# Optimization experiments

Hardware: AMD Instinct MI355X
Metric: run time of the kernel (lower is better)

Reference implementation:

```python
import jax, jax.numpy as jnp
import numpy as np

B = 262144          # flattened batch of (sample, time) points
D = 16              # input_dim: number of independent per-dimension MLPs
TE = 3              # time_embedding_dim -> per-dim MLP input width = 1 + TE = 4
H = 64              # hidden width (model_dims = [64, 64, 1])


def setup_inputs() -> dict:
    key = jax.random.key(0)
    ks = jax.random.split(key, 8)
    s1 = 1.0 / np.sqrt(1 + TE)   # torch nn.Linear default init scale ~ U(-1/sqrt(fan_in), ...)
    s2 = 1.0 / np.sqrt(H)
    return {
        "t": jax.random.normal(ks[0], (B, TE), jnp.float32),
        "y": jax.random.normal(ks[1], (B, D), jnp.float32),
        # stacked per-dim weights: layer l weight [D, in_l, out_l], bias [D, out_l]
        "W1": jax.random.uniform(ks[2], (D, 1 + TE, H), jnp.float32, -s1, s1),
        "b1": jax.random.uniform(ks[3], (D, H), jnp.float32, -s1, s1),
        "W2": jax.random.uniform(ks[4], (D, H, H), jnp.float32, -s2, s2),
        "b2": jax.random.uniform(ks[5], (D, H), jnp.float32, -s2, s2),
        "W3": jax.random.uniform(ks[6], (D, H, 1), jnp.float32, -s2, s2),
        "b3": jax.random.uniform(ks[7], (D, 1), jnp.float32, -s2, s2),
    }


def reference(t, y, W1, b1, W2, b2, W3, b3):
    # Per-dim MLP input: concat([y_i, t]) -> [B, D, 1+TE]
    Bn, Dn = y.shape
    x = jnp.concatenate(
        [y[:, :, None], jnp.broadcast_to(t[:, None, :], (Bn, Dn, t.shape[-1]))], axis=-1
    )
    h = jax.nn.softplus(jnp.einsum("bdi,dih->bdh", x, W1) + b1)      # Linear + Softplus
    h = jax.nn.softplus(jnp.einsum("bdh,dhk->bdk", h, W2) + b2)      # Linear + Softplus
    out = jnp.einsum("bdk,dko->bdo", h, W3) + b3                      # final Linear, out=1
    # concat over D then final activation: [B, D]
    return jax.nn.softplus(out[..., 0])
```

## Files before the change

kernel.cpp:

```cpp
#include <hip/hip_runtime.h>
#include <cmath>

#define B_TOTAL 262144
#define D 16
#define TE 3
#define H 64

#define TPB 16
#define NBX (B_TOTAL / 16 / TPB)
#define NBY 4

#define LOG2E 1.44269504088896340736f
#define LN2   0.693147180559945309417f

#define RSH 72
#define ARS 10

#define OSTRIDE (TPB * 16 * 4)

typedef _Float16 half8  __attribute__((ext_vector_type(8)));
typedef _Float16 half4  __attribute__((ext_vector_type(4)));
typedef __fp16   fp16x2 __attribute__((ext_vector_type(2)));
typedef float    f32x4  __attribute__((ext_vector_type(4)));
typedef unsigned int uint32;

__device__ __forceinline__ float sp_log2(float xs) {
    return __builtin_amdgcn_logf(1.0f + __builtin_amdgcn_exp2f(xs));
}
__device__ __forceinline__ float softplus_full(float x) {
    float e = __builtin_amdgcn_exp2f(-fabsf(x) * LOG2E);
    return fmaxf(x, 0.0f) + LN2 * __builtin_amdgcn_logf(1.0f + e);
}

__global__ __launch_bounds__(256, 4) void DiagonalVariance_kernel(
    const float* __restrict__ t,
    const float* __restrict__ y,
    const float* __restrict__ W1,
    const float* __restrict__ b1,
    const float* __restrict__ W2,
    const float* __restrict__ b2,
    const float* __restrict__ W3,
    const float* __restrict__ b3,
    float* __restrict__ out)
{
    __shared__ __align__(16) _Float16 tbuf[4 * 16 * RSH];
    __shared__ __align__(16) float obuf[2 * OSTRIDE];
    __shared__ __align__(16) uint32 abuf[256 * ARS];

    const int wave = threadIdx.x >> 6;
    const int lane = threadIdx.x & 63;
    const int q    = lane >> 4;
    const int lm   = lane & 15;
    const int d    = blockIdx.y * 4 + wave;
    const bool q0  = (q == 0);

    {
        const int i    = threadIdx.x;
        const int grow = blockIdx.x * 256 + i;
        const f32x4 yv = *(const f32x4*)(y + grow * D + blockIdx.y * 4);
        const float* tpp = t + grow * TE;
        const float tt0 = tpp[0], tt1 = tpp[1], tt2 = tpp[2];
        const uint32 u1 = __builtin_bit_cast(uint32, __builtin_amdgcn_cvt_pkrtz(tt1, tt2));
        uint32* ab = abuf + i * ARS;
        ab[0] = __builtin_bit_cast(uint32, __builtin_amdgcn_cvt_pkrtz(yv.x, tt0)); ab[1] = u1;
        ab[2] = __builtin_bit_cast(uint32, __builtin_amdgcn_cvt_pkrtz(yv.y, tt0)); ab[3] = u1;
        ab[4] = __builtin_bit_cast(uint32, __builtin_amdgcn_cvt_pkrtz(yv.z, tt0)); ab[5] = u1;
        ab[6] = __builtin_bit_cast(uint32, __builtin_amdgcn_cvt_pkrtz(yv.w, tt0)); ab[7] = u1;
    }

    const float* __restrict__ W1d = W1 + d * (4 * H);
    const float* __restrict__ b1d = b1 + d * H;
    const float* __restrict__ W2d = W2 + d * (H * H);
    const float* __restrict__ b2d = b2 + d * H;
    const float* __restrict__ W3d = W3 + d * H;

    half8 w2f[2][4];
    #pragma unroll
    for (int ks = 0; ks < 2; ++ks)
        #pragma unroll
        for (int nt = 0; nt < 4; ++nt)
            #pragma unroll
            for (int j = 0; j < 8; ++j)
                w2f[ks][nt][j] = (_Float16)W2d[(32 * ks + 8 * q + j) * H + 16 * nt + lm];

    half4 w1f[4];
    #pragma unroll
    for (int nt = 0; nt < 4; ++nt) {
        #pragma unroll
        for (int i = 0; i < 4; ++i) {
            const int h = 16 * nt + lm;
            float v = 0.0f;
            if (q == 0)           v = W1d[i * H + h] * LOG2E;
            if (q == 1 && i == 0) v = b1d[h] * LOG2E;
            w1f[nt][i] = (_Float16)v;
        }
    }

    const f32x4 ZC = {0.f, 0.f, 0.f, 0.f};
    f32x4 b2c[4];
    #pragma unroll
    for (int nt = 0; nt < 4; ++nt) {
        f32x4 bv = *(const f32x4*)(b2d + 16 * nt + 4 * q);
        b2c[nt] = (f32x4){bv.x * LOG2E, bv.y * LOG2E, bv.z * LOG2E, bv.w * LOG2E};
    }

    f32x4 w3l[4];
    #pragma unroll
    for (int nt = 0; nt < 4; ++nt) {
        f32x4 wv = *(const f32x4*)(W3d + 16 * nt + 4 * q);
        w3l[nt] = (f32x4){wv.x * LN2, wv.y * LN2, wv.z * LN2, wv.w * LN2};
    }

    const float sInit = ((lane & 48) == 0) ? b3[d] : 0.0f;

    _Float16* const tb  = tbuf + wave * (16 * RSH);
    _Float16* const twr = tb + (q * 4) * RSH + lm;
    const _Float16* const trd = tb + lm * RSH + 8 * q;

    const uint32* const ard = abuf + lm * ARS + 2 * wave;

    __syncthreads();

    uint32 a0n = ard[0];
    uint32 a1n = ard[1];

    #pragma unroll 1
    for (int tg = 0; tg < TPB; ++tg) {
        const uint32 a0 = a0n;
        const uint32 a1 = a1n;
        {
            const int tn = (tg + 1 < TPB) ? (tg + 1) : tg;
            a0n = ard[tn * 16 * ARS + 0];
            a1n = ard[tn * 16 * ARS + 1];
        }
        union { half4 h; uint32 u[2]; } af;
        af.u[0] = q0 ? a0 : 0x00003C00u;
        af.u[1] = q0 ? a1 : 0u;

        f32x4 acc1[4];
        #pragma unroll
        for (int nt = 0; nt < 4; ++nt)
            acc1[nt] = __builtin_amdgcn_mfma_f32_16x16x16f16(af.h, w1f[nt], ZC, 0, 0, 0);

        #pragma unroll
        for (int nt = 0; nt < 4; ++nt) {
            const fp16x2 p01 = __builtin_amdgcn_cvt_pkrtz(sp_log2(acc1[nt][0]),
                                                          sp_log2(acc1[nt][1]));
            const fp16x2 p23 = __builtin_amdgcn_cvt_pkrtz(sp_log2(acc1[nt][2]),
                                                          sp_log2(acc1[nt][3]));
            __fp16* const wb = (__fp16*)(twr + nt * 16);
            wb[0 * RSH] = p01.x;
            wb[1 * RSH] = p01.y;
            wb[2 * RSH] = p23.x;
            wb[3 * RSH] = p23.y;
        }

        half8 a2[2];
        #pragma unroll
        for (int ks = 0; ks < 2; ++ks)
            a2[ks] = *(const half8*)(trd + 32 * ks);

        f32x4 acc2[4];
        #pragma unroll
        for (int nt = 0; nt < 4; ++nt)
            acc2[nt] = __builtin_amdgcn_mfma_f32_16x16x32_f16(w2f[0][nt], a2[0], b2c[nt], 0, 0, 0);
        #pragma unroll
        for (int nt = 0; nt < 4; ++nt)
            acc2[nt] = __builtin_amdgcn_mfma_f32_16x16x32_f16(w2f[1][nt], a2[1], acc2[nt], 0, 0, 0);

        float s0 = sInit, s1 = 0.0f;
        #pragma unroll
        for (int nt = 0; nt < 4; ++nt) {
            s0 = fmaf(sp_log2(acc2[nt][0]), w3l[nt][0], s0);
            s1 = fmaf(sp_log2(acc2[nt][1]), w3l[nt][1], s1);
            s0 = fmaf(sp_log2(acc2[nt][2]), w3l[nt][2], s0);
            s1 = fmaf(sp_log2(acc2[nt][3]), w3l[nt][3], s1);
        }
        float s = s0 + s1;
        const uint32 sw = (uint32)__builtin_amdgcn_ds_swizzle(
            (int)__builtin_bit_cast(uint32, s), 0x401F);
        s += __builtin_bit_cast(float, sw);
        if ((lane & 16) == 0)
            obuf[(lane >> 5) * OSTRIDE + (tg * 16 + lm) * 4 + wave] = s;
    }

    __syncthreads();
    const int i = threadIdx.x;
    const f32x4 va = *(const f32x4*)(obuf + 4 * i);
    const f32x4 vb = *(const f32x4*)(obuf + OSTRIDE + 4 * i);
    f32x4 v;
    v.x = softplus_full(va.x + vb.x);
    v.y = softplus_full(va.y + vb.y);
    v.z = softplus_full(va.z + vb.z);
    v.w = softplus_full(va.w + vb.w);
    *(f32x4*)(out + (blockIdx.x * 256 + i) * D + blockIdx.y * 4) = v;
}

extern "C" void kernel_launch(void* const* d_in, const int* in_sizes, int n_in,
                              void* d_out, int out_size, void* d_ws, size_t ws_size,
                              hipStream_t stream) {
    const float* t  = (const float*)d_in[0];
    const float* y  = (const float*)d_in[1];
    const float* W1 = (const float*)d_in[2];
    const float* b1 = (const float*)d_in[3];
    const float* W2 = (const float*)d_in[4];
    const float* b2 = (const float*)d_in[5];
    const float* W3 = (const float*)d_in[6];
    const float* b3 = (const float*)d_in[7];
    float* out = (float*)d_out;

    DiagonalVariance_kernel<<<dim3(NBX, NBY), dim3(256), 0, stream>>>(
        t, y, W1, b1, W2, b2, W3, b3, out);
}
```

Before: 192.6 us.

## Keep layer-1 activations in registers by transposing MFMA to remove LDS round-trip

Layer 1 now computes the transposed product (weights as A, inputs as B), so each lane's accumulator output already sits in the B-operand layout a 16x16x16 MFMA expects. The hidden activations are packed to fp16 in registers and fed straight into layer 2, which removes the per-iteration LDS write/read through tbuf along with that buffer. Layer 2 moves from 8 K=32 MFMAs to 16 K=16 MFMAs, with W2 re-laid out to match. The trade-off is more MFMA issues per tile in exchange for dropping the shared-memory traffic and its waits.

```diff
diff --git a/kernel.cpp b/kernel.cpp
--- a/kernel.cpp
+++ b/kernel.cpp
@@ -13,7 +13,6 @@
 #define LOG2E 1.44269504088896340736f
 #define LN2   0.693147180559945309417f
 
-#define RSH 72
 #define ARS 10
 
 #define OSTRIDE (TPB * 16 * 4)
@@ -43,7 +42,6 @@
     const float* __restrict__ b3,
     float* __restrict__ out)
 {
-    __shared__ __align__(16) _Float16 tbuf[4 * 16 * RSH];
     __shared__ __align__(16) float obuf[2 * OSTRIDE];
     __shared__ __align__(16) uint32 abuf[256 * ARS];
 
@@ -74,15 +72,6 @@
     const float* __restrict__ b2d = b2 + d * H;
     const float* __restrict__ W3d = W3 + d * H;
 
-    half8 w2f[2][4];
-    #pragma unroll
-    for (int ks = 0; ks < 2; ++ks)
-        #pragma unroll
-        for (int nt = 0; nt < 4; ++nt)
-            #pragma unroll
-            for (int j = 0; j < 8; ++j)
-                w2f[ks][nt][j] = (_Float16)W2d[(32 * ks + 8 * q + j) * H + 16 * nt + lm];
-
     half4 w1f[4];
     #pragma unroll
     for (int nt = 0; nt < 4; ++nt) {
@@ -96,6 +85,15 @@
         }
     }
 
+    half4 w2a[4][4];
+    #pragma unroll
+    for (int c = 0; c < 4; ++c)
+        #pragma unroll
+        for (int nt = 0; nt < 4; ++nt)
+            #pragma unroll
+            for (int i = 0; i < 4; ++i)
+                w2a[c][nt][i] = (_Float16)W2d[(16 * c + 4 * q + i) * H + 16 * nt + lm];
+
     const f32x4 ZC = {0.f, 0.f, 0.f, 0.f};
     f32x4 b2c[4];
     #pragma unroll
@@ -112,10 +110,6 @@
     }
 
     const float sInit = ((lane & 48) == 0) ? b3[d] : 0.0f;
-
-    _Float16* const tb  = tbuf + wave * (16 * RSH);
-    _Float16* const twr = tb + (q * 4) * RSH + lm;
-    const _Float16* const trd = tb + lm * RSH + 8 * q;
 
     const uint32* const ard = abuf + lm * ARS + 2 * wave;
 
@@ -139,34 +133,27 @@
 
         f32x4 acc1[4];
         #pragma unroll
+        for (int c = 0; c < 4; ++c)
+            acc1[c] = __builtin_amdgcn_mfma_f32_16x16x16f16(w1f[c], af.h, ZC, 0, 0, 0);
+
+        union { half4 h; uint32 u[2]; } hb[4];
+        #pragma unroll
+        for (int c = 0; c < 4; ++c) {
+            hb[c].u[0] = __builtin_bit_cast(uint32,
+                __builtin_amdgcn_cvt_pkrtz(sp_log2(acc1[c][0]), sp_log2(acc1[c][1])));
+            hb[c].u[1] = __builtin_bit_cast(uint32,
+                __builtin_amdgcn_cvt_pkrtz(sp_log2(acc1[c][2]), sp_log2(acc1[c][3])));
+        }
+
+        f32x4 acc2[4];
+        #pragma unroll
         for (int nt = 0; nt < 4; ++nt)
-            acc1[nt] = __builtin_amdgcn_mfma_f32_16x16x16f16(af.h, w1f[nt], ZC, 0, 0, 0);
-
-        #pragma unroll
-        for (int nt = 0; nt < 4; ++nt) {
-            const fp16x2 p01 = __builtin_amdgcn_cvt_pkrtz(sp_log2(acc1[nt][0]),
-                                                          sp_log2(acc1[nt][1]));
-            const fp16x2 p23 = __builtin_amdgcn_cvt_pkrtz(sp_log2(acc1[nt][2]),
-                                                          sp_log2(acc1[nt][3]));
-            __fp16* const wb = (__fp16*)(twr + nt * 16);
-            wb[0 * RSH] = p01.x;
-            wb[1 * RSH] = p01.y;
-            wb[2 * RSH] = p23.x;
-            wb[3 * RSH] = p23.y;
-        }
-
-        half8 a2[2];
-        #pragma unroll
-        for (int ks = 0; ks < 2; ++ks)
-            a2[ks] = *(const half8*)(trd + 32 * ks);
-
-        f32x4 acc2[4];
-        #pragma unroll
-        for (int nt = 0; nt < 4; ++nt)
-            acc2[nt] = __builtin_amdgcn_mfma_f32_16x16x32_f16(w2f[0][nt], a2[0], b2c[nt], 0, 0, 0);
-        #pragma unroll
-        for (int nt = 0; nt < 4; ++nt)
-            acc2[nt] = __builtin_amdgcn_mfma_f32_16x16x32_f16(w2f[1][nt], a2[1], acc2[nt], 0, 0, 0);
+            acc2[nt] = __builtin_amdgcn_mfma_f32_16x16x16f16(w2a[0][nt], hb[0].h, b2c[nt], 0, 0, 0);
+        #pragma unroll
+        for (int c = 1; c < 4; ++c)
+            #pragma unroll
+            for (int nt = 0; nt < 4; ++nt)
+                acc2[nt] = __builtin_amdgcn_mfma_f32_16x16x16f16(w2a[c][nt], hb[c].h, acc2[nt], 0, 0, 0);
 
         float s0 = sInit, s1 = 0.0f;
         #pragma unroll
```

After: 188.4 us. 2.1% less time.
